# Kernel tuning notes

Hardware: AMD Instinct MI355X
Metric: run time of the kernel (lower is better)

Reference implementation:

```python
import jax, jax.numpy as jnp
import numpy as np
import math

DIM_V = 512

def setup_inputs() -> dict:
    key = jax.random.key(0)
    k1, k2, k3, k4, k5, k6 = jax.random.split(key, 6)
    B, C, N, M = 8, DIM_V, 4096, 1024
    pcd_up = jax.random.normal(k1, (B, C, N), dtype=jnp.float32)
    pcd_down = jax.random.normal(k2, (B, C, M), dtype=jnp.float32)
    s = 1.0 / math.sqrt(C)
    Wq = jax.random.normal(k3, (C, C), dtype=jnp.float32) * s
    Wk = jax.random.normal(k4, (C, C), dtype=jnp.float32) * s
    Wv = jax.random.normal(k5, (C, C), dtype=jnp.float32) * s
    Wskip = jax.random.normal(k6, (C, C), dtype=jnp.float32) * s
    return {"pcd_up": pcd_up, "pcd_down": pcd_down, "Wq": Wq, "Wk": Wk, "Wv": Wv, "Wskip": Wskip}

def reference(pcd_up, pcd_down, Wq, Wk, Wv, Wskip):
    # 1x1 Conv1d == per-point linear: weight [out_c, in_c]
    q = jnp.einsum('oc,bcn->bon', Wq, pcd_up)      # [B, C, N]
    k = jnp.einsum('oc,bcm->bom', Wk, pcd_down)    # [B, C, M]
    v = jnp.einsum('oc,bcm->bom', Wv, pcd_down)    # [B, C, M]
    C = q.shape[1]
    scale = jnp.sqrt(jnp.asarray(C, dtype=q.dtype))  # sqrt(q.shape[-2]) = sqrt(C)
    energy = jnp.einsum('bcn,bcm->bnm', q, k) / scale  # [B, N, M]
    attention = jax.nn.softmax(energy, axis=-1)
    x = jnp.einsum('bnm,bcm->bcn', attention, v)       # [B, C, N]
    skip = jnp.einsum('oc,bcn->bon', Wskip, pcd_up)
    return skip + x
```

## Files before the change

kernel.cpp:

```cpp
#include <hip/hip_runtime.h>
#include <cstddef>

#define Bn 8
#define Cd 512
#define Nn 4096
#define Mm 1024

typedef __attribute__((ext_vector_type(8))) short s8v;
typedef __attribute__((ext_vector_type(4))) float v4f;
typedef __attribute__((ext_vector_type(16))) float v16f;

__device__ __forceinline__ float b2f(unsigned short u) {
    union { unsigned int i; float f; } v; v.i = ((unsigned int)u) << 16; return v.f;
}
__device__ __forceinline__ unsigned short f2b(float f) {
    union { float f; unsigned int i; } v; v.f = f;
    unsigned int x = v.i;
    unsigned int r = (x + 0x7FFFu + ((x >> 16) & 1u)) >> 16;
    return (unsigned short)r;
}
__device__ __forceinline__ v4f mfma16(s8v a, s8v b, v4f c) {
    return __builtin_amdgcn_mfma_f32_16x16x32_bf16(a, b, c, 0, 0, 0);
}
__device__ __forceinline__ v16f mfma32(s8v a, s8v b, v16f c) {
    return __builtin_amdgcn_mfma_f32_32x32x16_bf16(a, b, c, 0, 0, 0);
}
__device__ __forceinline__ void gload_lds16(const unsigned short* gsrc, unsigned char* lds) {
    __builtin_amdgcn_global_load_lds(
        (const __attribute__((address_space(1))) unsigned int*)gsrc,
        (__attribute__((address_space(3))) unsigned int*)lds, 16, 0, 0);
}

__global__ __launch_bounds__(256) void convwf(const float* __restrict__ Wq, const float* __restrict__ Wk,
                                              const float* __restrict__ Wv, const float* __restrict__ Ws,
                                              unsigned short* __restrict__ Wf) {
    const float* S = (blockIdx.y == 0) ? Wq : (blockIdx.y == 1) ? Wk : (blockIdx.y == 2) ? Wv : Ws;
    const int o16 = blockIdx.x;
    const int t = threadIdx.x;
    const int l = t & 63, sub = t >> 6;
    const int lq = l & 15, quad = l >> 4;
    unsigned short* dst = Wf + (size_t)blockIdx.y * 262144;
#pragma unroll
    for (int rep = 0; rep < 4; ++rep) {
        int cstep = sub * 4 + rep;
        const float* src = S + (size_t)(o16 * 16 + lq) * Cd + cstep * 32 + quad * 8;
        float4 va = *(const float4*)(src);
        float4 vb = *(const float4*)(src + 4);
        union { ushort4 h[2]; uint4 q; } pk;
        pk.h[0].x = f2b(va.x); pk.h[0].y = f2b(va.y); pk.h[0].z = f2b(va.z); pk.h[0].w = f2b(va.w);
        pk.h[1].x = f2b(vb.x); pk.h[1].y = f2b(vb.y); pk.h[1].z = f2b(vb.z); pk.h[1].w = f2b(vb.w);
        *(uint4*)(dst + ((size_t)(o16 * 16 + cstep) * 64 + l) * 8) = pk.q;
    }
}

__global__ __launch_bounds__(256) void convx(const float* __restrict__ X,
                                             unsigned short* __restrict__ Xt,
                                             int Nx) {
    __shared__ float Lf[64][65];
    const int t = threadIdx.x;
    const int b = blockIdx.z, c0 = blockIdx.y * 64;
    const int nl0 = blockIdx.x * 64;
    const int cl = t >> 4, n4 = (t & 15) * 4;
    const float* Xb = X + (size_t)b * Cd * Nx + nl0;
#pragma unroll
    for (int cc = 0; cc < 4; ++cc) {
        int c = cc * 16 + cl;
        float4 v = *(const float4*)(Xb + (size_t)(c0 + c) * Nx + n4);
        Lf[n4 + 0][c] = v.x; Lf[n4 + 1][c] = v.y;
        Lf[n4 + 2][c] = v.z; Lf[n4 + 3][c] = v.w;
    }
    __syncthreads();
    unsigned short* Xtb = Xt + ((size_t)b * Nx + nl0) * Cd + c0;
#pragma unroll
    for (int rep = 0; rep < 2; ++rep) {
        int u = t + rep * 256;
        int n = u >> 3, c8 = (u & 7) * 8;
        union { ushort4 h[2]; uint4 q; } pk;
        pk.h[0].x = f2b(Lf[n][c8 + 0]); pk.h[0].y = f2b(Lf[n][c8 + 1]);
        pk.h[0].z = f2b(Lf[n][c8 + 2]); pk.h[0].w = f2b(Lf[n][c8 + 3]);
        pk.h[1].x = f2b(Lf[n][c8 + 4]); pk.h[1].y = f2b(Lf[n][c8 + 5]);
        pk.h[1].z = f2b(Lf[n][c8 + 6]); pk.h[1].w = f2b(Lf[n][c8 + 7]);
        *(uint4*)(Xtb + (size_t)n * Cd + c8) = pk.q;
    }
}

template <int PAIRB>
__global__ __launch_bounds__(256, 2) void gemm4(const unsigned short* __restrict__ Wf,
                                                unsigned short* XY,
                                                unsigned short* __restrict__ Y2,
                                                float* __restrict__ outF,
                                                int Nc) {
    __shared__ __align__(16) unsigned char raw[PAIRB ? 34816 : 8192];
    const int t = threadIdx.x;
    const int l = t & 63, w = t >> 6, lq = t & 15, quad = (t >> 4) & 3;
    const int bid = blockIdx.x;
    const int b = bid & 7, n0 = (bid >> 3) * 32;
    unsigned short* Xb = XY + ((size_t)b * Nc + n0) * Cd;
    const unsigned short* W1f = Wf + (size_t)(PAIRB ? 0 : 1) * 262144 + (size_t)l * 8;
    const unsigned short* W2f = Wf + (size_t)(PAIRB ? 3 : 2) * 262144 + (size_t)l * 8;

    v4f acc1[8][2], acc2[8][2];
#pragma unroll
    for (int i = 0; i < 8; ++i)
#pragma unroll
        for (int nt = 0; nt < 2; ++nt) {
            acc1[i][nt] = (v4f){0.f, 0.f, 0.f, 0.f};
            acc2[i][nt] = (v4f){0.f, 0.f, 0.f, 0.f};
        }

#define STAGE4(s, c0)                                                            \
    if (t < 128) gload_lds16(Xb + (size_t)(t >> 2) * Cd + (c0) + (t & 3) * 8,    \
                             raw + (s) * 2048 + t * 16);

    STAGE4(0, 0);
    for (int step = 0; step < 16; ++step) {
        const int c0 = step * 32, cur = step & 1;
        __syncthreads();
        s8v a1[8], a2[8];
#pragma unroll
        for (int i = 0; i < 8; ++i)
            a1[i] = *(const s8v*)(W1f + ((size_t)((w * 8 + i) * 16 + step) << 9));
#pragma unroll
        for (int i = 0; i < 8; ++i)
            a2[i] = *(const s8v*)(W2f + ((size_t)((w * 8 + i) * 16 + step) << 9));
        if (step < 15) { STAGE4(cur ^ 1, c0 + 32) }
        const short* Xs = (const short*)(raw + cur * 2048);
        s8v bf0 = *(const s8v*)(Xs + lq * 32 + quad * 8);
        s8v bf1 = *(const s8v*)(Xs + (lq + 16) * 32 + quad * 8);
#pragma unroll
        for (int i = 0; i < 8; ++i) {
            acc1[i][0] = mfma16(a1[i], bf0, acc1[i][0]);
            acc1[i][1] = mfma16(a1[i], bf1, acc1[i][1]);
        }
#pragma unroll
        for (int i = 0; i < 8; ++i) {
            acc2[i][0] = mfma16(a2[i], bf0, acc2[i][0]);
            acc2[i][1] = mfma16(a2[i], bf1, acc2[i][1]);
        }
    }
#undef STAGE4
    __syncthreads();

    if (PAIRB) {
#pragma unroll
        for (int i = 0; i < 8; ++i)
#pragma unroll
            for (int nt = 0; nt < 2; ++nt)
#pragma unroll
                for (int r = 0; r < 4; ++r) {
                    int o = (w * 8 + i) * 16 + quad * 4 + r;
                    int n = n0 + nt * 16 + lq;
                    outF[((size_t)b * Cd + o) * Nn + n] = acc2[i][nt][r];
                }
        short (*T2)[528] = reinterpret_cast<short(*)[528]>(raw);
#pragma unroll
        for (int i = 0; i < 8; ++i)
#pragma unroll
            for (int nt = 0; nt < 2; ++nt)
#pragma unroll
                for (int r = 0; r < 4; ++r)
                    T2[nt * 16 + lq][(w * 8 + i) * 16 + quad * 4 + r] = (short)f2b(acc1[i][nt][r]);
        __syncthreads();
        {
            int row = t >> 3, cb = (t & 7) * 64;
            unsigned short* qp = Xb + (size_t)row * Cd + cb;
#pragma unroll
            for (int j = 0; j < 8; ++j)
                *(uint4*)(qp + j * 8) = *(const uint4*)(&T2[row][cb + j * 8]);
        }
    } else {
        const int half = quad >> 1, ebase = (quad & 1) * 4;
        {
            unsigned short* Kb = XY + (size_t)b * Mm * Cd;
            const int mt = n0 >> 5;
#pragma unroll
            for (int i = 0; i < 8; ++i) {
                int kb = w * 8 + i;
#pragma unroll
                for (int nt = 0; nt < 2; ++nt) {
                    int lf = (nt * 16 + lq) + 32 * half;
                    ushort4 v;
                    v.x = f2b(acc1[i][nt][0]); v.y = f2b(acc1[i][nt][1]);
                    v.z = f2b(acc1[i][nt][2]); v.w = f2b(acc1[i][nt][3]);
                    *(ushort4*)(Kb + ((size_t)(mt * 32 + kb) * 64 + lf) * 8 + ebase) = v;
                }
            }
        }
        short (*Vst)[40] = reinterpret_cast<short(*)[40]>(raw + w * 1280);
        unsigned short* Vb0 = Y2 + (size_t)b * Cd * Mm;
#pragma unroll
        for (int i = 0; i < 8; ++i) {
#pragma unroll
            for (int nt = 0; nt < 2; ++nt)
#pragma unroll
                for (int r = 0; r < 4; ++r)
                    Vst[quad * 4 + r][nt * 16 + lq] = (short)f2b(acc2[i][nt][r]);
            int c_abs = (w * 8 + i) * 16 + (l >> 2);
            int m8 = l & 3;
            int ct = c_abs >> 5, mb = (n0 >> 4) + (m8 >> 1);
            int lf = (c_abs & 31) + 32 * (m8 & 1);
            uint4 v = *(const uint4*)(&Vst[l >> 2][m8 * 8]);
            *(uint4*)(Vb0 + ((size_t)(ct * 64 + mb) * 64 + lf) * 8) = v;
        }
    }
}

template <int MODE>
__global__ __launch_bounds__(256) void gemm_mfma(const float* __restrict__ W,
                                                 const float* __restrict__ X,
                                                 float* __restrict__ Yf,
                                                 unsigned short* __restrict__ Yb,
                                                 int Nx) {
    __shared__ short Xs[64][40];
    __shared__ short Tt[16][72];
    const int t = threadIdx.x;
    const int w = t >> 6, lq = t & 15, quad = (t >> 4) & 3;
    const int b = blockIdx.z, o0 = blockIdx.y * 64, n0 = blockIdx.x * 64;
    const float* Xb = X + (size_t)b * Cd * Nx;
    const float* Wrow = W + (size_t)(o0 + w * 16 + lq) * Cd;

    v4f acc[4];
#pragma unroll
    for (int i = 0; i < 4; ++i) acc[i] = (v4f){0.f, 0.f, 0.f, 0.f};

    for (int c0 = 0; c0 < Cd; c0 += 32) {
#pragma unroll
        for (int p = 0; p < 2; ++p) {
            int i = t + p * 256;
            int c = i >> 4;
            int n4 = (i & 15) * 4;
            float4 x = *(const float4*)(Xb + (size_t)(c0 + c) * Nx + n0 + n4);
            Xs[n4 + 0][c] = (short)f2b(x.x); Xs[n4 + 1][c] = (short)f2b(x.y);
            Xs[n4 + 2][c] = (short)f2b(x.z); Xs[n4 + 3][c] = (short)f2b(x.w);
        }
        union { unsigned short h[8]; s8v s; } af;
        {
            float4 wa = *(const float4*)(Wrow + c0 + quad * 8);
            float4 wb = *(const float4*)(Wrow + c0 + quad * 8 + 4);
            af.h[0] = f2b(wa.x); af.h[1] = f2b(wa.y); af.h[2] = f2b(wa.z); af.h[3] = f2b(wa.w);
            af.h[4] = f2b(wb.x); af.h[5] = f2b(wb.y); af.h[6] = f2b(wb.z); af.h[7] = f2b(wb.w);
        }
        __syncthreads();
#pragma unroll
        for (int nt = 0; nt < 4; ++nt) {
            s8v bf = *(const s8v*)(&Xs[nt * 16 + lq][quad * 8]);
            acc[nt] = mfma16(af.s, bf, acc[nt]);
        }
        __syncthreads();
    }

    if (MODE == 0) {
#pragma unroll
        for (int nt = 0; nt < 4; ++nt)
#pragma unroll
            for (int r = 0; r < 4; ++r) {
                int o = o0 + w * 16 + quad * 4 + r;
                int n = n0 + nt * 16 + lq;
                Yf[((size_t)b * Cd + o) * Nx + n] = acc[nt][r];
            }
    } else {
#pragma unroll
        for (int nt = 0; nt < 4; ++nt) {
#pragma unroll
            for (int r = 0; r < 4; ++r)
                Tt[lq][w * 16 + quad * 4 + r] = (short)f2b(acc[nt][r]);
            __syncthreads();
            int nrow = t >> 4, o4 = (t & 15) * 4;
            ushort4 val = *(const ushort4*)(&Tt[nrow][o4]);
            *(ushort4*)(Yb + ((size_t)b * Nx + n0 + nt * 16 + nrow) * Cd + o0 + o4) = val;
            __syncthreads();
        }
    }
}

__global__ __launch_bounds__(512, 2) void attn_v3(const unsigned short* __restrict__ Qt,
                                                  const unsigned short* __restrict__ Kf,
                                                  const unsigned short* __restrict__ Vf,
                                                  float* __restrict__ out) {
    __shared__ __align__(16) unsigned char Ls[104192];
    unsigned char* Lq = Ls;
    unsigned short* Pb = (unsigned short*)(Ls + 65536);
    float* pmaxS  = (float*)(Ls + 99328);
    float* psumS  = (float*)(Ls + 101376);
    float* muS    = (float*)(Ls + 103424);
    float* ssumS  = (float*)(Ls + 103680);
    float* alphaS = (float*)(Ls + 103936);
    float* OtA    = (float*)Ls;

    const int t = threadIdx.x;
    const int l = t & 63, w = t >> 6;
    const int lcol = l & 31, lhalf = l >> 5;
    const int bid = blockIdx.x;
    const int b = bid & 7, n0 = (bid >> 3) * 64;

    {
        const unsigned short* qb = Qt + ((size_t)b * Nn + n0) * Cd;
#pragma unroll
        for (int i = 0; i < 8; ++i) {
            int s = i * 512 + t;
            int n = s >> 6, u = s & 63;
            uint4 v = *(const uint4*)(qb + (size_t)n * Cd + u * 8);
            *(uint4*)(Lq + ((n * 64 + (u ^ (n & 15))) << 4)) = v;
        }
    }
    if (t < 64) { muS[t] = -1e30f; ssumS[t] = 0.f; }

    v16f o_acc[2][2];
#pragma unroll
    for (int nh = 0; nh < 2; ++nh)
#pragma unroll
        for (int ti = 0; ti < 2; ++ti)
#pragma unroll
            for (int r = 0; r < 16; ++r) o_acc[nh][ti][r] = 0.f;
    __syncthreads();

    const unsigned short* Kfb = Kf + (size_t)b * Mm * Cd + (size_t)l * 8;
    const unsigned short* Vfb = Vf + (size_t)b * Cd * Mm + (size_t)l * 8;
    const int q0 = lcol * 64, q1 = (lcol + 32) * 64;
    const int swz = lcol & 15;
    const float sc = 0.04419417382415922f;

    for (int m0 = 0; m0 < Mm; m0 += 256) {
        v16f st0, st1;
#pragma unroll
        for (int r = 0; r < 16; ++r) { st0[r] = 0.f; st1[r] = 0.f; }
        const unsigned short* kp = Kfb + (size_t)(((m0 >> 5) + w) * 32) * 512;
#pragma unroll
        for (int kb8 = 0; kb8 < 4; ++kb8) {
            uint4 ka[8];
#pragma unroll
            for (int j = 0; j < 8; ++j) ka[j] = *(const uint4*)(kp + (size_t)(kb8 * 8 + j) * 512);
            __builtin_amdgcn_s_setprio(1);
#pragma unroll
            for (int j = 0; j < 8; ++j) {
                int kb = kb8 * 8 + j;
                int uo = (kb * 2 + lhalf) ^ swz;
                s8v qf0 = *(const s8v*)(Lq + ((q0 + uo) << 4));
                s8v qf1 = *(const s8v*)(Lq + ((q1 + uo) << 4));
                union { uint4 u; s8v s; } av; av.u = ka[j];
                st0 = mfma32(av.s, qf0, st0);
                st1 = mfma32(av.s, qf1, st1);
            }
            __builtin_amdgcn_s_setprio(0);
        }
        uint4 v0p[8];
        {
            const unsigned short* vc = Vfb + (size_t)((w * 2) * 64 + (m0 >> 4)) * 512;
#pragma unroll
            for (int j = 0; j < 8; ++j) v0p[j] = *(const uint4*)(vc + (size_t)j * 512);
        }
#pragma unroll
        for (int r = 0; r < 16; ++r) { st0[r] *= sc; st1[r] *= sc; }
        float tm0 = st0[0], tm1 = st1[0];
#pragma unroll
        for (int r = 1; r < 16; ++r) { tm0 = fmaxf(tm0, st0[r]); tm1 = fmaxf(tm1, st1[r]); }
        tm0 = fmaxf(tm0, __shfl_xor(tm0, 32));
        tm1 = fmaxf(tm1, __shfl_xor(tm1, 32));
        if (l < 32) {
            pmaxS[l * 8 + w] = tm0;
            pmaxS[(l + 32) * 8 + w] = tm1;
        }
        __syncthreads();
        {
            int row = t >> 3, p = t & 7;
            float v = pmaxS[row * 8 + p];
            v = fmaxf(v, __shfl_xor(v, 1));
            v = fmaxf(v, __shfl_xor(v, 2));
            v = fmaxf(v, __shfl_xor(v, 4));
            if (p == 0) {
                float mold = muS[row];
                float mx = fmaxf(mold, v);
                alphaS[row] = __expf(mold - mx);
                muS[row] = mx;
            }
        }
        __syncthreads();
        {
            float mx0 = muS[lcol], mx1 = muS[lcol + 32];
            float e0[16], e1[16], rs0 = 0.f, rs1 = 0.f;
#pragma unroll
            for (int r = 0; r < 16; ++r) {
                e0[r] = __expf(st0[r] - mx0); rs0 += e0[r];
                e1[r] = __expf(st1[r] - mx1); rs1 += e1[r];
            }
            rs0 += __shfl_xor(rs0, 32);
            rs1 += __shfl_xor(rs1, 32);
            if (l < 32) {
                psumS[l * 8 + w] = rs0;
                psumS[(l + 32) * 8 + w] = rs1;
            }
#pragma unroll
            for (int rg = 0; rg < 4; ++rg) {
                ushort4 pk0, pk1;
                pk0.x = f2b(e0[rg * 4 + 0]); pk0.y = f2b(e0[rg * 4 + 1]);
                pk0.z = f2b(e0[rg * 4 + 2]); pk0.w = f2b(e0[rg * 4 + 3]);
                pk1.x = f2b(e1[rg * 4 + 0]); pk1.y = f2b(e1[rg * 4 + 1]);
                pk1.z = f2b(e1[rg * 4 + 2]); pk1.w = f2b(e1[rg * 4 + 3]);
                *(ushort4*)(Pb + lcol * 264 + w * 32 + 8 * rg + 4 * lhalf) = pk0;
                *(ushort4*)(Pb + (lcol + 32) * 264 + w * 32 + 8 * rg + 4 * lhalf) = pk1;
            }
        }
        __syncthreads();
        {
            int row = t >> 3, p = t & 7;
            float v = psumS[row * 8 + p];
            v += __shfl_xor(v, 1);
            v += __shfl_xor(v, 2);
            v += __shfl_xor(v, 4);
            if (p == 0) ssumS[row] = ssumS[row] * alphaS[row] + v;
        }

        float ar0[16], ar1[16];
#pragma unroll
        for (int r = 0; r < 16; ++r) {
            int crow = (r & 3) + 8 * (r >> 2) + 4 * lhalf;
            ar0[r] = alphaS[crow];
            ar1[r] = alphaS[32 + crow];
        }
#pragma unroll
        for (int ti = 0; ti < 2; ++ti)
#pragma unroll
            for (int r = 0; r < 16; ++r) {
                o_acc[0][ti][r] *= ar0[r];
                o_acc[1][ti][r] *= ar1[r];
            }

#pragma unroll
        for (int h = 0; h < 2; ++h) {
            s8v pA0[8], pA1[8];
#pragma unroll
            for (int j = 0; j < 8; ++j) {
                pA0[j] = *(const s8v*)(Pb + lcol * 264 + (h * 8 + j) * 16 + lhalf * 8);
                pA1[j] = *(const s8v*)(Pb + (lcol + 32) * 264 + (h * 8 + j) * 16 + lhalf * 8);
            }
#pragma unroll
            for (int ti = 0; ti < 2; ++ti) {
                uint4 vb[8];
                if (h == 0 && ti == 0) {
#pragma unroll
                    for (int j = 0; j < 8; ++j) vb[j] = v0p[j];
                } else {
                    const unsigned short* vc = Vfb + (size_t)((w * 2 + ti) * 64 + (m0 >> 4) + h * 8) * 512;
#pragma unroll
                    for (int j = 0; j < 8; ++j) vb[j] = *(const uint4*)(vc + (size_t)j * 512);
                }
                __builtin_amdgcn_s_setprio(1);
#pragma unroll
                for (int j = 0; j < 8; ++j) {
                    union { uint4 u; s8v s; } bv; bv.u = vb[j];
                    o_acc[0][ti] = mfma32(pA0[j], bv.s, o_acc[0][ti]);
                    o_acc[1][ti] = mfma32(pA1[j], bv.s, o_acc[1][ti]);
                }
                __builtin_amdgcn_s_setprio(0);
            }
        }
        __syncthreads();
    }

    float inv0[16], inv1[16];
#pragma unroll
    for (int r = 0; r < 16; ++r) {
        int crow = (r & 3) + 8 * (r >> 2) + 4 * lhalf;
        inv0[r] = 1.0f / ssumS[crow];
        inv1[r] = 1.0f / ssumS[32 + crow];
    }
    float* OtW = OtA + w * 32 * 36;
#pragma unroll
    for (int nh = 0; nh < 2; ++nh)
#pragma unroll
        for (int ti = 0; ti < 2; ++ti) {
#pragma unroll
            for (int r = 0; r < 16; ++r) {
                int crow = (r & 3) + 8 * (r >> 2) + 4 * lhalf;
                OtW[lcol * 36 + crow] = o_acc[nh][ti][r] * (nh ? inv1[r] : inv0[r]);
            }
            int cloc = l >> 1, half = l & 1;
            int cabs = (w * 2 + ti) * 32 + cloc;
            const float* src = OtW + cloc * 36 + half * 16;
            float* op = out + ((size_t)b * Cd + cabs) * Nn + n0 + nh * 32 + half * 16;
#pragma unroll
            for (int j = 0; j < 4; ++j) {
                float4 a = *(const float4*)(src + j * 4);
                float4 g = *(const float4*)(op + j * 4);
                g.x += a.x; g.y += a.y; g.z += a.z; g.w += a.w;
                *(float4*)(op + j * 4) = g;
            }
        }
}

__device__ __forceinline__ float u2lo(unsigned int u) {
    union { unsigned int i; float f; } v; v.i = u << 16; return v.f;
}
__device__ __forceinline__ float u2hi(unsigned int u) {
    union { unsigned int i; float f; } v; v.i = u & 0xFFFF0000u; return v.f;
}

__global__ __launch_bounds__(256) void attn_k(const float* __restrict__ up,
                                              const float* __restrict__ Wq,
                                              const unsigned short* __restrict__ Ktb,
                                              const unsigned short* __restrict__ Vtb,
                                              float* __restrict__ out) {
    __shared__ float Qs[16][516];
    __shared__ __align__(16) unsigned char Sraw[24576];
    unsigned short (*Us)[16]  = reinterpret_cast<unsigned short(*)[16]>(Sraw);
    unsigned short (*Wt)[512] = reinterpret_cast<unsigned short(*)[512]>(Sraw + 16384);
    float (*Ps)[65] = reinterpret_cast<float(*)[65]>(Sraw);
    float* mu_s     = reinterpret_cast<float*>(Sraw + 4160);
    float* ssum_s   = reinterpret_cast<float*>(Sraw + 4224);
    float* alpha_s  = reinterpret_cast<float*>(Sraw + 4288);

    const int t = threadIdx.x;
    const int b = blockIdx.y;
    const int n0 = blockIdx.x * 16;
    const int row = t & 15;
    const int grp = t >> 4;

    for (int i = t; i < Cd * 16; i += 256) {
        int c = i >> 4, r = i & 15;
        Us[c][r] = f2b(up[((size_t)b * Cd + c) * Nn + n0 + r]);
    }
    __syncthreads();

    float acc[32];
#pragma unroll
    for (int j = 0; j < 32; ++j) acc[j] = 0.f;

    for (int k0 = 0; k0 < Cd; k0 += 8) {
        for (int i = t; i < 1024; i += 256) {
            int oc = i >> 1;
            int kc = (i & 1) * 4;
            float4 wv = *(const float4*)(Wq + (size_t)oc * Cd + k0 + kc);
            Wt[kc + 0][oc] = f2b(wv.x); Wt[kc + 1][oc] = f2b(wv.y);
            Wt[kc + 2][oc] = f2b(wv.z); Wt[kc + 3][oc] = f2b(wv.w);
        }
        __syncthreads();
#pragma unroll
        for (int k = 0; k < 8; ++k) {
            float u = b2f(Us[k0 + k][row]);
            const ushort4* wr = (const ushort4*)(&Wt[k][grp * 32]);
#pragma unroll
            for (int j4 = 0; j4 < 8; ++j4) {
                ushort4 wv = wr[j4];
                acc[j4 * 4 + 0] += u * b2f(wv.x);
                acc[j4 * 4 + 1] += u * b2f(wv.y);
                acc[j4 * 4 + 2] += u * b2f(wv.z);
                acc[j4 * 4 + 3] += u * b2f(wv.w);
            }
        }
        __syncthreads();
    }

    const float scale = 0.04419417382415922f;
#pragma unroll
    for (int j = 0; j < 32; ++j) Qs[row][grp * 32 + j] = acc[j] * scale;
    if (t < 16) { mu_s[t] = -1e30f; ssum_s[t] = 0.f; }
#pragma unroll
    for (int j = 0; j < 32; ++j) acc[j] = 0.f;
    __syncthreads();

    const float4* qr = (const float4*)(&Qs[row][0]);

    for (int m0 = 0; m0 < Mm; m0 += 64) {
        {
            int mb = m0 + grp * 4;
            const uint4* K0 = (const uint4*)(Ktb + ((size_t)b * Mm + mb + 0) * Cd);
            const uint4* K1 = (const uint4*)(Ktb + ((size_t)b * Mm + mb + 1) * Cd);
            const uint4* K2 = (const uint4*)(Ktb + ((size_t)b * Mm + mb + 2) * Cd);
            const uint4* K3 = (const uint4*)(Ktb + ((size_t)b * Mm + mb + 3) * Cd);
            float a0 = 0.f, a1 = 0.f, a2 = 0.f, a3 = 0.f;
#pragma unroll 4
            for (int c8 = 0; c8 < Cd / 8; ++c8) {
                float4 qa = qr[2 * c8], qb = qr[2 * c8 + 1];
                uint4 k0v = K0[c8], k1v = K1[c8], k2v = K2[c8], k3v = K3[c8];
                a0 += qa.x * u2lo(k0v.x) + qa.y * u2hi(k0v.x) + qa.z * u2lo(k0v.y) + qa.w * u2hi(k0v.y)
                    + qb.x * u2lo(k0v.z) + qb.y * u2hi(k0v.z) + qb.z * u2lo(k0v.w) + qb.w * u2hi(k0v.w);
                a1 += qa.x * u2lo(k1v.x) + qa.y * u2hi(k1v.x) + qa.z * u2lo(k1v.y) + qa.w * u2hi(k1v.y)
                    + qb.x * u2lo(k1v.z) + qb.y * u2hi(k1v.z) + qb.z * u2lo(k1v.w) + qb.w * u2hi(k1v.w);
                a2 += qa.x * u2lo(k2v.x) + qa.y * u2hi(k2v.x) + qa.z * u2lo(k2v.y) + qa.w * u2hi(k2v.y)
                    + qb.x * u2lo(k2v.z) + qb.y * u2hi(k2v.z) + qb.z * u2lo(k2v.w) + qb.w * u2hi(k2v.w);
                a3 += qa.x * u2lo(k3v.x) + qa.y * u2hi(k3v.x) + qa.z * u2lo(k3v.y) + qa.w * u2hi(k3v.y)
                    + qb.x * u2lo(k3v.z) + qb.y * u2hi(k3v.z) + qb.z * u2lo(k3v.w) + qb.w * u2hi(k3v.w);
            }
            Ps[row][grp * 4 + 0] = a0;
            Ps[row][grp * 4 + 1] = a1;
            Ps[row][grp * 4 + 2] = a2;
            Ps[row][grp * 4 + 3] = a3;
        }
        __syncthreads();
        if (t < 16) {
            float mold = mu_s[t];
            float mx = mold;
            for (int m = 0; m < 64; ++m) mx = fmaxf(mx, Ps[t][m]);
            float al = __expf(mold - mx);
            float s = ssum_s[t] * al;
            for (int m = 0; m < 64; ++m) {
                float p = __expf(Ps[t][m] - mx);
                Ps[t][m] = p;
                s += p;
            }
            mu_s[t] = mx; ssum_s[t] = s; alpha_s[t] = al;
        }
        __syncthreads();
        {
            float arr = alpha_s[row];
#pragma unroll
            for (int j = 0; j < 32; ++j) acc[j] *= arr;
            const unsigned short* Vbase = Vtb + (size_t)b * Mm * Cd + (size_t)grp * 32;
            for (int m = 0; m < 64; ++m) {
                float p = Ps[row][m];
                const uint4* vr = (const uint4*)(Vbase + (size_t)(m0 + m) * Cd);
#pragma unroll
                for (int j4 = 0; j4 < 4; ++j4) {
                    uint4 v = vr[j4];
                    acc[j4 * 8 + 0] += p * u2lo(v.x); acc[j4 * 8 + 1] += p * u2hi(v.x);
                    acc[j4 * 8 + 2] += p * u2lo(v.y); acc[j4 * 8 + 3] += p * u2hi(v.y);
                    acc[j4 * 8 + 4] += p * u2lo(v.z); acc[j4 * 8 + 5] += p * u2hi(v.z);
                    acc[j4 * 8 + 6] += p * u2lo(v.w); acc[j4 * 8 + 7] += p * u2hi(v.w);
                }
            }
        }
        __syncthreads();
    }

    float invv = 1.0f / ssum_s[row];
#pragma unroll
    for (int j = 0; j < 32; ++j) {
        int c = grp * 32 + j;
        size_t idx = ((size_t)b * Cd + c) * Nn + n0 + row;
        out[idx] = out[idx] + acc[j] * invv;
    }
}

extern "C" void kernel_launch(void* const* d_in, const int* in_sizes, int n_in,
                              void* d_out, int out_size, void* d_ws, size_t ws_size,
                              hipStream_t stream) {
    const float* up   = (const float*)d_in[0];
    const float* down = (const float*)d_in[1];
    const float* Wq   = (const float*)d_in[2];
    const float* Wk   = (const float*)d_in[3];
    const float* Wv   = (const float*)d_in[4];
    const float* Wsk  = (const float*)d_in[5];
    float* out = (float*)d_out;

    const size_t szK = (size_t)Bn * Mm * Cd;
    const size_t szQ = (size_t)Bn * Nn * Cd;
    const size_t szW = (size_t)4 * Cd * Cd;

    if (ws_size >= (2 * szK + szQ + szW) * 2) {
        unsigned short* XK = (unsigned short*)d_ws;
        unsigned short* Vf = XK + szK;
        unsigned short* XQ = Vf + szK;
        unsigned short* Wf = XQ + szQ;
        convwf<<<dim3(32, 4), 256, 0, stream>>>(Wq, Wk, Wv, Wsk, Wf);
        convx<<<dim3(Mm / 64, Cd / 64, Bn), 256, 0, stream>>>(down, XK, Mm);
        gemm4<0><<<dim3(Bn * (Mm / 32)), 256, 0, stream>>>(Wf, XK, Vf, nullptr, Mm);
        convx<<<dim3(Nn / 64, Cd / 64, Bn), 256, 0, stream>>>(up, XQ, Nn);
        gemm4<1><<<dim3(Bn * (Nn / 32)), 256, 0, stream>>>(Wf, XQ, nullptr, out, Nn);
        attn_v3<<<dim3((Nn / 64) * Bn), 512, 0, stream>>>(XQ, XK, Vf, out);
    } else {
        unsigned short* Ktb = (unsigned short*)d_ws;
        unsigned short* Vtb = Ktb + szK;
        gemm_mfma<2><<<dim3(Mm / 64, Cd / 64, Bn), 256, 0, stream>>>(Wk, down, nullptr, Ktb, Mm);
        gemm_mfma<2><<<dim3(Mm / 64, Cd / 64, Bn), 256, 0, stream>>>(Wv, down, nullptr, Vtb, Mm);
        gemm_mfma<0><<<dim3(Nn / 64, Cd / 64, Bn), 256, 0, stream>>>(Wsk, up, out, nullptr, Nn);
        attn_k<<<dim3(Nn / 16, Bn), 256, 0, stream>>>(up, Wq, Ktb, Vtb, out);
    }
}
```

Baseline: 324.2 us.

## Fuse Q and skip projections into the attention kernel prologue

Removes the separate convx and gemm4<1> launches for pcd_up. The attention kernel now loads fp32 up directly, converts it to bf16 into swizzled LDS, and computes the Q projection and skip projection with MFMA. It writes skip to the output and puts bf16 Q back into LDS for the attention loop. This saves a workspace round trip for Q and two launches, but each attention block now carries a heavier prologue, with uncoalesced 2-byte LDS stores and weight loads from global memory.

```diff
diff --git a/kernel.cpp b/kernel.cpp
--- a/kernel.cpp
+++ b/kernel.cpp
@@ -90,14 +90,14 @@
                                                 unsigned short* __restrict__ Y2,
                                                 float* __restrict__ outF,
                                                 int Nc) {
-    __shared__ __align__(16) unsigned char raw[PAIRB ? 34816 : 8192];
+    __shared__ __align__(16) unsigned char raw[8192];
     const int t = threadIdx.x;
     const int l = t & 63, w = t >> 6, lq = t & 15, quad = (t >> 4) & 3;
     const int bid = blockIdx.x;
     const int b = bid & 7, n0 = (bid >> 3) * 32;
     unsigned short* Xb = XY + ((size_t)b * Nc + n0) * Cd;
-    const unsigned short* W1f = Wf + (size_t)(PAIRB ? 0 : 1) * 262144 + (size_t)l * 8;
-    const unsigned short* W2f = Wf + (size_t)(PAIRB ? 3 : 2) * 262144 + (size_t)l * 8;
+    const unsigned short* W1f = Wf + (size_t)1 * 262144 + (size_t)l * 8;
+    const unsigned short* W2f = Wf + (size_t)2 * 262144 + (size_t)l * 8;
 
     v4f acc1[8][2], acc2[8][2];
 #pragma unroll
@@ -141,67 +141,38 @@
 #undef STAGE4
     __syncthreads();
 
-    if (PAIRB) {
-#pragma unroll
-        for (int i = 0; i < 8; ++i)
-#pragma unroll
-            for (int nt = 0; nt < 2; ++nt)
-#pragma unroll
-                for (int r = 0; r < 4; ++r) {
-                    int o = (w * 8 + i) * 16 + quad * 4 + r;
-                    int n = n0 + nt * 16 + lq;
-                    outF[((size_t)b * Cd + o) * Nn + n] = acc2[i][nt][r];
-                }
-        short (*T2)[528] = reinterpret_cast<short(*)[528]>(raw);
-#pragma unroll
-        for (int i = 0; i < 8; ++i)
-#pragma unroll
-            for (int nt = 0; nt < 2; ++nt)
-#pragma unroll
-                for (int r = 0; r < 4; ++r)
-                    T2[nt * 16 + lq][(w * 8 + i) * 16 + quad * 4 + r] = (short)f2b(acc1[i][nt][r]);
-        __syncthreads();
-        {
-            int row = t >> 3, cb = (t & 7) * 64;
-            unsigned short* qp = Xb + (size_t)row * Cd + cb;
-#pragma unroll
-            for (int j = 0; j < 8; ++j)
-                *(uint4*)(qp + j * 8) = *(const uint4*)(&T2[row][cb + j * 8]);
-        }
-    } else {
-        const int half = quad >> 1, ebase = (quad & 1) * 4;
-        {
-            unsigned short* Kb = XY + (size_t)b * Mm * Cd;
-            const int mt = n0 >> 5;
-#pragma unroll
-            for (int i = 0; i < 8; ++i) {
-                int kb = w * 8 + i;
-#pragma unroll
-                for (int nt = 0; nt < 2; ++nt) {
-                    int lf = (nt * 16 + lq) + 32 * half;
-                    ushort4 v;
-                    v.x = f2b(acc1[i][nt][0]); v.y = f2b(acc1[i][nt][1]);
-                    v.z = f2b(acc1[i][nt][2]); v.w = f2b(acc1[i][nt][3]);
-                    *(ushort4*)(Kb + ((size_t)(mt * 32 + kb) * 64 + lf) * 8 + ebase) = v;
-                }
-            }
-        }
-        short (*Vst)[40] = reinterpret_cast<short(*)[40]>(raw + w * 1280);
-        unsigned short* Vb0 = Y2 + (size_t)b * Cd * Mm;
+    const int half = quad >> 1, ebase = (quad & 1) * 4;
+    {
+        unsigned short* Kb = XY + (size_t)b * Mm * Cd;
+        const int mt = n0 >> 5;
 #pragma unroll
         for (int i = 0; i < 8; ++i) {
-#pragma unroll
-            for (int nt = 0; nt < 2; ++nt)
-#pragma unroll
-                for (int r = 0; r < 4; ++r)
-                    Vst[quad * 4 + r][nt * 16 + lq] = (short)f2b(acc2[i][nt][r]);
-            int c_abs = (w * 8 + i) * 16 + (l >> 2);
-            int m8 = l & 3;
-            int ct = c_abs >> 5, mb = (n0 >> 4) + (m8 >> 1);
-            int lf = (c_abs & 31) + 32 * (m8 & 1);
-            uint4 v = *(const uint4*)(&Vst[l >> 2][m8 * 8]);
-            *(uint4*)(Vb0 + ((size_t)(ct * 64 + mb) * 64 + lf) * 8) = v;
-        }
+            int kb = w * 8 + i;
+#pragma unroll
+            for (int nt = 0; nt < 2; ++nt) {
+                int lf = (nt * 16 + lq) + 32 * half;
+                ushort4 v;
+                v.x = f2b(acc1[i][nt][0]); v.y = f2b(acc1[i][nt][1]);
+                v.z = f2b(acc1[i][nt][2]); v.w = f2b(acc1[i][nt][3]);
+                *(ushort4*)(Kb + ((size_t)(mt * 32 + kb) * 64 + lf) * 8 + ebase) = v;
+            }
+        }
+    }
+    short (*Vst)[40] = reinterpret_cast<short(*)[40]>(raw + w * 1280);
+    unsigned short* Vb0 = Y2 + (size_t)b * Cd * Mm;
+#pragma unroll
+    for (int i = 0; i < 8; ++i) {
+#pragma unroll
+        for (int nt = 0; nt < 2; ++nt)
+#pragma unroll
+            for (int r = 0; r < 4; ++r)
+                Vst[quad * 4 + r][nt * 16 + lq] = (short)f2b(acc2[i][nt][r]);
+        int c_abs = (w * 8 + i) * 16 + (l >> 2);
+        int m8 = l & 3;
+        int ct = c_abs >> 5, mb = (n0 >> 4) + (m8 >> 1);
+        int lf = (c_abs & 31) + 32 * (m8 & 1);
+        uint4 v = *(const uint4*)(&Vst[l >> 2][m8 * 8]);
+        *(uint4*)(Vb0 + ((size_t)(ct * 64 + mb) * 64 + lf) * 8) = v;
     }
 }
 
@@ -273,10 +244,11 @@
     }
 }
 
-__global__ __launch_bounds__(512, 2) void attn_v3(const unsigned short* __restrict__ Qt,
-                                                  const unsigned short* __restrict__ Kf,
-                                                  const unsigned short* __restrict__ Vf,
-                                                  float* __restrict__ out) {
+__global__ __launch_bounds__(512, 2) void attn_f(const float* __restrict__ up,
+                                                 const unsigned short* __restrict__ Wf,
+                                                 const unsigned short* __restrict__ Kf,
+                                                 const unsigned short* __restrict__ Vf,
+                                                 float* __restrict__ out) {
     __shared__ __align__(16) unsigned char Ls[104192];
     unsigned char* Lq = Ls;
     unsigned short* Pb = (unsigned short*)(Ls + 65536);
@@ -290,18 +262,80 @@
     const int t = threadIdx.x;
     const int l = t & 63, w = t >> 6;
     const int lcol = l & 31, lhalf = l >> 5;
+    const int lq = l & 15, quad = (l >> 4) & 3;
     const int bid = blockIdx.x;
     const int b = bid & 7, n0 = (bid >> 3) * 64;
 
     {
-        const unsigned short* qb = Qt + ((size_t)b * Nn + n0) * Cd;
-#pragma unroll
-        for (int i = 0; i < 8; ++i) {
-            int s = i * 512 + t;
-            int n = s >> 6, u = s & 63;
-            uint4 v = *(const uint4*)(qb + (size_t)n * Cd + u * 8);
-            *(uint4*)(Lq + ((n * 64 + (u ^ (n & 15))) << 4)) = v;
-        }
+        const float* ub = up + (size_t)b * Cd * Nn + n0;
+#pragma unroll
+        for (int it = 0; it < 16; ++it) {
+            int i = it * 512 + t;
+            int c = i >> 4, n4 = (i & 15) * 4;
+            float4 v = *(const float4*)(ub + (size_t)c * Nn + n4);
+            int cu = c >> 3, ce = (c & 7) * 2;
+            float vv[4] = {v.x, v.y, v.z, v.w};
+#pragma unroll
+            for (int j = 0; j < 4; ++j) {
+                int n = n4 + j;
+                *(unsigned short*)(Lq + ((n * 64 + (cu ^ (n & 15))) << 4) + ce) = f2b(vv[j]);
+            }
+        }
+    }
+    __syncthreads();
+
+    {
+        v4f aq[4][4], ask[4][4];
+#pragma unroll
+        for (int oi = 0; oi < 4; ++oi)
+#pragma unroll
+            for (int ni = 0; ni < 4; ++ni) {
+                aq[oi][ni] = (v4f){0.f, 0.f, 0.f, 0.f};
+                ask[oi][ni] = (v4f){0.f, 0.f, 0.f, 0.f};
+            }
+        const unsigned short* WqF = Wf + (size_t)l * 8;
+        const unsigned short* WsF = Wf + (size_t)3 * 262144 + (size_t)l * 8;
+        for (int step = 0; step < 16; ++step) {
+            s8v a1[4], a2[4];
+#pragma unroll
+            for (int oi = 0; oi < 4; ++oi)
+                a1[oi] = *(const s8v*)(WqF + ((size_t)((w * 4 + oi) * 16 + step) << 9));
+#pragma unroll
+            for (int oi = 0; oi < 4; ++oi)
+                a2[oi] = *(const s8v*)(WsF + ((size_t)((w * 4 + oi) * 16 + step) << 9));
+#pragma unroll
+            for (int ni = 0; ni < 4; ++ni) {
+                int n = ni * 16 + lq;
+                s8v bf = *(const s8v*)(Lq + ((n * 64 + ((step * 4 + quad) ^ lq)) << 4));
+#pragma unroll
+                for (int oi = 0; oi < 4; ++oi) {
+                    aq[oi][ni] = mfma16(a1[oi], bf, aq[oi][ni]);
+                    ask[oi][ni] = mfma16(a2[oi], bf, ask[oi][ni]);
+                }
+            }
+        }
+#pragma unroll
+        for (int oi = 0; oi < 4; ++oi)
+#pragma unroll
+            for (int ni = 0; ni < 4; ++ni)
+#pragma unroll
+                for (int r = 0; r < 4; ++r) {
+                    int o = w * 64 + oi * 16 + quad * 4 + r;
+                    int n = n0 + ni * 16 + lq;
+                    out[((size_t)b * Cd + o) * Nn + n] = ask[oi][ni][r];
+                }
+        __syncthreads();
+#pragma unroll
+        for (int oi = 0; oi < 4; ++oi)
+#pragma unroll
+            for (int ni = 0; ni < 4; ++ni) {
+                int n = ni * 16 + lq;
+                int cu = w * 8 + oi * 2 + (quad >> 1);
+                ushort4 pk;
+                pk.x = f2b(aq[oi][ni][0]); pk.y = f2b(aq[oi][ni][1]);
+                pk.z = f2b(aq[oi][ni][2]); pk.w = f2b(aq[oi][ni][3]);
+                *(ushort4*)(Lq + ((n * 64 + (cu ^ lq)) << 4) + (quad & 1) * 8) = pk;
+            }
     }
     if (t < 64) { muS[t] = -1e30f; ssumS[t] = 0.f; }
 
@@ -643,20 +677,16 @@
     float* out = (float*)d_out;
 
     const size_t szK = (size_t)Bn * Mm * Cd;
-    const size_t szQ = (size_t)Bn * Nn * Cd;
     const size_t szW = (size_t)4 * Cd * Cd;
 
-    if (ws_size >= (2 * szK + szQ + szW) * 2) {
+    if (ws_size >= (2 * szK + szW) * 2) {
         unsigned short* XK = (unsigned short*)d_ws;
         unsigned short* Vf = XK + szK;
-        unsigned short* XQ = Vf + szK;
-        unsigned short* Wf = XQ + szQ;
+        unsigned short* Wf = Vf + szK;
         convwf<<<dim3(32, 4), 256, 0, stream>>>(Wq, Wk, Wv, Wsk, Wf);
         convx<<<dim3(Mm / 64, Cd / 64, Bn), 256, 0, stream>>>(down, XK, Mm);
         gemm4<0><<<dim3(Bn * (Mm / 32)), 256, 0, stream>>>(Wf, XK, Vf, nullptr, Mm);
-        convx<<<dim3(Nn / 64, Cd / 64, Bn), 256, 0, stream>>>(up, XQ, Nn);
-        gemm4<1><<<dim3(Bn * (Nn / 32)), 256, 0, stream>>>(Wf, XQ, nullptr, out, Nn);
-        attn_v3<<<dim3((Nn / 64) * Bn), 512, 0, stream>>>(XQ, XK, Vf, out);
+        attn_f<<<dim3((Nn / 64) * Bn), 512, 0, stream>>>(up, Wf, XK, Vf, out);
     } else {
         unsigned short* Ktb = (unsigned short*)d_ws;
         unsigned short* Vtb = Ktb + szK;
```

Measured after the change: 281.4 us. -13.2%, faster.
